# Kernel tuning notes

Hardware: AMD Instinct MI355X
Metric: run time of the kernel (lower is better)

## Reference

```python
import jax, jax.numpy as jnp
import numpy as np

B, L, DM, H, PD = 2, 1024, 512, 8, 64
D = DM // H  # head_dim = 64
NEG = -10000.0


def setup_inputs() -> dict:
    key = jax.random.key(0)
    ks = jax.random.split(key, 12)
    s = 1.0 / np.sqrt(DM)
    sp = 1.0 / np.sqrt(PD)
    return {
        "x": jax.random.normal(ks[0], (B, L, DM), dtype=jnp.float32),
        "z": jax.random.normal(ks[1], (B, L, L, PD), dtype=jnp.float32),
        "residue_mask": jnp.ones((B, L), dtype=bool),
        "Wq": jax.random.normal(ks[2], (DM, DM), dtype=jnp.float32) * s,
        "bq": jnp.zeros((DM,), dtype=jnp.float32),
        "Wk": jax.random.normal(ks[3], (DM, DM), dtype=jnp.float32) * s,
        "bk": jnp.zeros((DM,), dtype=jnp.float32),
        "Wv": jax.random.normal(ks[4], (DM, DM), dtype=jnp.float32) * s,
        "bv": jnp.zeros((DM,), dtype=jnp.float32),
        "Wo": jax.random.normal(ks[5], (DM, DM), dtype=jnp.float32) * s,
        "bo": jnp.zeros((DM,), dtype=jnp.float32),
        "Wpb": jax.random.normal(ks[6], (PD, H), dtype=jnp.float32) * sp,
    }


def reference(x, z, residue_mask, Wq, bq, Wk, bk, Wv, bv, Wo, bo, Wpb):
    b, l, c = x.shape
    scale = 1.0 / np.sqrt(D)
    # projections -> (B, H, L, D)
    q = (x @ Wq + bq).reshape(b, l, H, D).transpose(0, 2, 1, 3)
    k = (x @ Wk + bk).reshape(b, l, H, D).transpose(0, 2, 1, 3)
    v = (x @ Wv + bv).reshape(b, l, H, D).transpose(0, 2, 1, 3)
    # pair bias: (B, L, L, PD) @ (PD, H) -> (B, H, L, L)
    bias = jnp.einsum('bijp,ph->bhij', z, Wpb)
    logits = jnp.einsum('bhid,bhjd->bhij', q, k) * scale + bias
    key_ok = residue_mask[:, None, None, :]
    query_ok = residue_mask[:, None, :, None]
    logits = jnp.where(key_ok, logits, NEG)
    logits = jnp.where(query_ok, logits, NEG)
    attn = jax.nn.softmax(logits, axis=-1)
    out = jnp.einsum('bhij,bhjd->bhid', attn, v)
    out = out.transpose(0, 2, 1, 3).reshape(b, l, c)
    return out @ Wo + bo
```

## Files before the change

kernel.cpp:

```cpp
#include <hip/hip_runtime.h>

typedef __bf16 bf16;
typedef __attribute__((ext_vector_type(4))) __bf16 bf16x4;
typedef __attribute__((ext_vector_type(8))) __bf16 bf16x8;
typedef __attribute__((ext_vector_type(4))) float f32x4;
typedef __attribute__((ext_vector_type(4))) _Float16 f16x4;
typedef __attribute__((ext_vector_type(2))) _Float16 f16x2;

#define B_   2
#define L_   1024
#define DM_  512
#define H_   8
#define D_   64
#define PD_  64
#define NEG_VAL -10000.0f

#define WTPB_N (16*64)

static __device__ __forceinline__ f32x4 mfma_bf16(bf16x8 a, bf16x8 b, f32x4 c) {
  return __builtin_amdgcn_mfma_f32_16x16x32_bf16(a, b, c, 0, 0, 0);
}

__global__ __launch_bounds__(256) void prep_kernel(
    const float* __restrict__ x, const float* __restrict__ Wq, const float* __restrict__ Wk,
    const float* __restrict__ Wv, const float* __restrict__ Wo, const float* __restrict__ Wpb,
    bf16* __restrict__ xb, bf16* __restrict__ Wt, bf16* __restrict__ Wto, bf16* __restrict__ Wtpb) {
  __shared__ float td[32][33];
  int bid = blockIdx.x, tid = threadIdx.x;
  if (bid < 1024) {
    int r = tid >> 3, c4 = (tid & 7) * 4;
    const float* src;
    bf16* dstbase;
    int n0, k0, srcol;
    if (bid < 768) {
      int nt2 = bid >> 4, kt = bid & 15;
      n0 = nt2 * 32; k0 = kt * 32;
      int sel = n0 >> 9;
      src = sel == 0 ? Wq : (sel == 1 ? Wk : Wv);
      srcol = n0 & 511;
      dstbase = Wt + (long)n0 * 512;
    } else {
      int t2 = bid - 768;
      int nt2 = t2 >> 4, kt = t2 & 15;
      n0 = nt2 * 32; k0 = kt * 32;
      src = Wo; srcol = n0;
      dstbase = Wto + (long)n0 * 512;
    }
    f32x4 v = *reinterpret_cast<const f32x4*>(src + (long)(k0 + r) * 512 + srcol + c4);
#pragma unroll
    for (int e = 0; e < 4; ++e) td[r][c4 + e] = v[e];
    __syncthreads();
    int nl = tid >> 3, k4 = (tid & 7) * 4;
    bf16x4 o;
#pragma unroll
    for (int e = 0; e < 4; ++e) o[e] = (bf16)td[k4 + e][nl];
    *reinterpret_cast<bf16x4*>(dstbase + (long)nl * 512 + k0 + k4) = o;
  } else if (bid < 2048) {
    int base = (bid - 1024) * 1024 + tid * 4;
    f32x4 v = *reinterpret_cast<const f32x4*>(x + base);
    bf16x4 o;
#pragma unroll
    for (int e = 0; e < 4; ++e) o[e] = (bf16)v[e];
    *reinterpret_cast<bf16x4*>(xb + base) = o;
  } else {
    for (int t = tid; t < WTPB_N; t += 256) {
      int n = t >> 6, kk = t & 63;
      Wtpb[t] = (n < 8) ? (bf16)Wpb[kk * 8 + n] : (bf16)0.0f;
    }
  }
}

__global__ __launch_bounds__(256) void qkv_gemm(
    const bf16* __restrict__ xb, const bf16* __restrict__ Wt,
    const float* __restrict__ bq, const float* __restrict__ bk, const float* __restrict__ bv,
    bf16* __restrict__ qb, bf16* __restrict__ kb, bf16* __restrict__ vT) {
  int wid = blockIdx.x * 4 + (threadIdx.x >> 6);
  int lane = threadIdx.x & 63;
  int mt = wid / 48, nt = wid - mt * 48;
  int row0 = mt * 32, col0 = nt * 32;
  int lr = lane & 15, lg = lane >> 4;
  const bf16* a0p = xb + (row0 + lr) * 512 + lg * 8;
  const bf16* a1p = a0p + 16 * 512;
  const bf16* b0p = Wt + (col0 + lr) * 512 + lg * 8;
  const bf16* b1p = b0p + 16 * 512;
  f32x4 acc00 = {0.f,0.f,0.f,0.f}, acc01 = acc00, acc10 = acc00, acc11 = acc00;
#pragma unroll
  for (int kk = 0; kk < 512; kk += 32) {
    bf16x8 a0 = *reinterpret_cast<const bf16x8*>(a0p + kk);
    bf16x8 a1 = *reinterpret_cast<const bf16x8*>(a1p + kk);
    bf16x8 b0 = *reinterpret_cast<const bf16x8*>(b0p + kk);
    bf16x8 b1 = *reinterpret_cast<const bf16x8*>(b1p + kk);
    acc00 = mfma_bf16(a0, b0, acc00);
    acc01 = mfma_bf16(a0, b1, acc01);
    acc10 = mfma_bf16(a1, b0, acc10);
    acc11 = mfma_bf16(a1, b1, acc11);
  }
#pragma unroll
  for (int ni = 0; ni < 2; ++ni) {
    int col = col0 + ni * 16 + lr;
    int wsel = col >> 9;
    int ncol = col & 511;
    int h = ncol >> 6, d = ncol & 63;
    const float* bias = wsel == 0 ? bq : (wsel == 1 ? bk : bv);
    float bval = bias[ncol];
#pragma unroll
    for (int mi = 0; mi < 2; ++mi) {
      f32x4 acc = (mi == 0) ? (ni == 0 ? acc00 : acc01) : (ni == 0 ? acc10 : acc11);
      int m0 = row0 + mi * 16 + lg * 4;
      int bidx = m0 >> 10, l0 = m0 & 1023;
      if (wsel == 2) {
        bf16x4 pv;
#pragma unroll
        for (int r = 0; r < 4; ++r) pv[r] = (bf16)(acc[r] + bval);
        *reinterpret_cast<bf16x4*>(vT + ((long)(bidx * H_ + h) * D_ + d) * L_ + l0) = pv;
      } else if (wsel == 0) {
#pragma unroll
        for (int r = 0; r < 4; ++r)
          qb[((long)(bidx * H_ + h) * L_ + l0 + r) * D_ + d] = (bf16)((acc[r] + bval) * 0.125f);
      } else {
#pragma unroll
        for (int r = 0; r < 4; ++r)
          kb[((long)(bidx * H_ + h) * L_ + l0 + r) * D_ + d] = (bf16)(acc[r] + bval);
      }
    }
  }
}

__global__ __launch_bounds__(256) void bias_gemm(
    const float* __restrict__ z, const bf16* __restrict__ Wtpb, const int* __restrict__ mask,
    _Float16* __restrict__ biasbuf) {
  __shared__ float zt_raw[64 * 64];
  __shared__ _Float16 bt[8][72];
  int tid = threadIdx.x;
  int w = tid >> 6, lane = tid & 63;
  int lr = lane & 15, lg = lane >> 4;
  char* zb = (char*)zt_raw;
  const char* zsrc = (const char*)(z + (long)blockIdx.x * 4096);
#pragma unroll
  for (int q = 0; q < 4; ++q) {
    int lb = q * 4096 + tid * 16;
    int row = lb >> 8, col = lb & 255;
    f32x4 v = *reinterpret_cast<const f32x4*>(zsrc + lb);
    *reinterpret_cast<f32x4*>(zb + row * 256 + (col ^ ((row & 7) << 5))) = v;
  }
  bf16x8 b0 = *reinterpret_cast<const bf16x8*>(Wtpb + lr * 64 + lg * 8);
  bf16x8 b1 = *reinterpret_cast<const bf16x8*>(Wtpb + lr * 64 + 32 + lg * 8);
  __syncthreads();
  int row = w * 16 + lr;
  int sw = (row & 7) << 5;
  const char* zr = zb + row * 256;
  f32x4 z0 = *reinterpret_cast<const f32x4*>(zr + ((lg * 32) ^ sw));
  f32x4 z1 = *reinterpret_cast<const f32x4*>(zr + (((lg * 32) ^ sw) + 16));
  f32x4 z2 = *reinterpret_cast<const f32x4*>(zr + ((128 + lg * 32) ^ sw));
  f32x4 z3 = *reinterpret_cast<const f32x4*>(zr + (((128 + lg * 32) ^ sw) + 16));
  bf16x8 a0, a1;
#pragma unroll
  for (int e = 0; e < 4; ++e) { a0[e] = (bf16)z0[e]; a0[e + 4] = (bf16)z1[e]; }
#pragma unroll
  for (int e = 0; e < 4; ++e) { a1[e] = (bf16)z2[e]; a1[e + 4] = (bf16)z3[e]; }
  f32x4 acc = {0.f, 0.f, 0.f, 0.f};
  acc = mfma_bf16(a0, b0, acc);
  acc = mfma_bf16(a1, b1, acc);
  __syncthreads();
  if (lr < 8) {
    f16x4 hv;
#pragma unroll
    for (int r = 0; r < 4; ++r) hv[r] = (_Float16)acc[r];
    *reinterpret_cast<f16x4*>(&bt[lr][w * 16 + lg * 4]) = hv;
  }
  __syncthreads();
  {
    int h = tid >> 5, part = tid & 31;
    long pb = (long)blockIdx.x * 64;
    int b = (int)(pb >> 20), i = ((int)(pb >> 10)) & 1023, j0 = (int)pb & 1023;
    int j = j0 + part * 2;
    f16x2 v = *reinterpret_cast<const f16x2*>(&bt[h][part * 2]);
    if (mask[b * L_ + j] == 0)     v[0] = (_Float16)NEG_VAL;
    if (mask[b * L_ + j + 1] == 0) v[1] = (_Float16)NEG_VAL;
    _Float16* dst = biasbuf + ((((long)b * H_ + h) * L_ + i) << 10) + j;
    *reinterpret_cast<f16x2*>(dst) = v;
  }
}

__global__ __launch_bounds__(256) void attn_kernel(
    const bf16* __restrict__ qb, const bf16* __restrict__ kb, const bf16* __restrict__ vT,
    const _Float16* __restrict__ biasb, const int* __restrict__ mask, bf16* __restrict__ attn_out) {
  __shared__ bf16 p_lds[4][16 * 64];
  __shared__ float o_lds[4][16][64];
  __shared__ float m_lds[4][16];
  __shared__ float l_lds[4][16];
  int bid = blockIdx.x;
  int b = bid >> 9, h = (bid >> 6) & 7, it = bid & 63;
  int i0 = it * 16;
  int tid = threadIdx.x, w = tid >> 6, lane = tid & 63, lr = lane & 15, lg = lane >> 4;

  const bf16* qrow = qb + ((long)(b * H_ + h) * L_ + i0 + lr) * D_ + lg * 8;
  bf16x8 qa0 = *reinterpret_cast<const bf16x8*>(qrow);
  bf16x8 qa1 = *reinterpret_cast<const bf16x8*>(qrow + 32);
  const bf16* kbase = kb + (long)(b * H_ + h) * L_ * D_;
  const bf16* vbase = vT + (long)(b * H_ + h) * D_ * L_;
  const _Float16* bias_base = biasb + ((long)(b * H_ + h) * L_ + i0) * L_;
  bool qok = mask[b * L_ + i0 + lr] != 0;

  float m = -3.0e38f, l = 0.f;
  f32x4 o0 = {0.f,0.f,0.f,0.f}, o1 = o0, o2 = o0, o3 = o0;
  char* pbuf = (char*)&p_lds[w][0];
  int swz = (lr & 7) << 4;

  for (int jt = 0; jt < 4; ++jt) {
    int j0 = w * 256 + jt * 64;
    f32x4 s0, s1, s2, s3;
#pragma unroll
    for (int tile = 0; tile < 4; ++tile) {
      f16x4 bv = *reinterpret_cast<const f16x4*>(bias_base + (long)lr * L_ + j0 + tile * 16 + lg * 4);
      f32x4 acc;
#pragma unroll
      for (int r = 0; r < 4; ++r) acc[r] = (float)bv[r];
      const bf16* kr = kbase + (long)(j0 + tile * 16 + lr) * D_ + lg * 8;
      acc = mfma_bf16(*reinterpret_cast<const bf16x8*>(kr), qa0, acc);
      acc = mfma_bf16(*reinterpret_cast<const bf16x8*>(kr + 32), qa1, acc);
      if (tile == 0) s0 = acc; else if (tile == 1) s1 = acc; else if (tile == 2) s2 = acc; else s3 = acc;
    }
    if (!qok) {
#pragma unroll
      for (int r = 0; r < 4; ++r) { s0[r] = NEG_VAL; s1[r] = NEG_VAL; s2[r] = NEG_VAL; s3[r] = NEG_VAL; }
    }
    float mt = s0[0];
#pragma unroll
    for (int r = 0; r < 4; ++r) mt = fmaxf(fmaxf(fmaxf(mt, s0[r]), fmaxf(s1[r], s2[r])), s3[r]);
    mt = fmaxf(mt, __shfl_xor(mt, 16));
    mt = fmaxf(mt, __shfl_xor(mt, 32));
    float mnew = fmaxf(m, mt);
    float alpha = __expf(m - mnew);
    m = mnew;
    f32x4 p0, p1, p2, p3;
    float ps = 0.f;
#pragma unroll
    for (int r = 0; r < 4; ++r) {
      p0[r] = __expf(s0[r] - mnew); p1[r] = __expf(s1[r] - mnew);
      p2[r] = __expf(s2[r] - mnew); p3[r] = __expf(s3[r] - mnew);
      ps += p0[r] + p1[r] + p2[r] + p3[r];
    }
    ps += __shfl_xor(ps, 16);
    ps += __shfl_xor(ps, 32);
    l = l * alpha + ps;
#pragma unroll
    for (int r = 0; r < 4; ++r) { o0[r] *= alpha; o1[r] *= alpha; o2[r] *= alpha; o3[r] *= alpha; }
#pragma unroll
    for (int tile = 0; tile < 4; ++tile) {
      f32x4 pv = (tile == 0) ? p0 : (tile == 1) ? p1 : (tile == 2) ? p2 : p3;
      bf16x4 pb_;
#pragma unroll
      for (int r = 0; r < 4; ++r) pb_[r] = (bf16)pv[r];
      *reinterpret_cast<bf16x4*>(pbuf + ((lr * 128 + tile * 32 + lg * 8) ^ swz)) = pb_;
    }
    bf16x8 pa0 = *reinterpret_cast<const bf16x8*>(pbuf + ((lr * 128 + lg * 16) ^ swz));
    bf16x8 pa1 = *reinterpret_cast<const bf16x8*>(pbuf + ((lr * 128 + 64 + lg * 16) ^ swz));
#pragma unroll
    for (int dtile = 0; dtile < 4; ++dtile) {
      const bf16* vr = vbase + (long)(dtile * 16 + lr) * L_ + j0 + lg * 8;
      f32x4 acc = (dtile == 0) ? o0 : (dtile == 1) ? o1 : (dtile == 2) ? o2 : o3;
      acc = mfma_bf16(*reinterpret_cast<const bf16x8*>(vr), pa0, acc);
      acc = mfma_bf16(*reinterpret_cast<const bf16x8*>(vr + 32), pa1, acc);
      if (dtile == 0) o0 = acc; else if (dtile == 1) o1 = acc; else if (dtile == 2) o2 = acc; else o3 = acc;
    }
  }
#pragma unroll
  for (int dtile = 0; dtile < 4; ++dtile) {
    f32x4 ov = (dtile == 0) ? o0 : (dtile == 1) ? o1 : (dtile == 2) ? o2 : o3;
    *reinterpret_cast<f32x4*>(&o_lds[w][lr][dtile * 16 + lg * 4]) = ov;
  }
  if (lg == 0) { m_lds[w][lr] = m; l_lds[w][lr] = l; }
  __syncthreads();
  {
    int row = tid >> 4, d0 = (tid & 15) * 4;
    float M = fmaxf(fmaxf(m_lds[0][row], m_lds[1][row]), fmaxf(m_lds[2][row], m_lds[3][row]));
    float lt = 0.f;
    float oacc[4] = {0.f, 0.f, 0.f, 0.f};
#pragma unroll
    for (int ww = 0; ww < 4; ++ww) {
      float c = __expf(m_lds[ww][row] - M);
      lt += c * l_lds[ww][row];
#pragma unroll
      for (int e = 0; e < 4; ++e) oacc[e] += c * o_lds[ww][row][d0 + e];
    }
    float inv = 1.0f / lt;
    bf16x4 ov;
#pragma unroll
    for (int e = 0; e < 4; ++e) ov[e] = (bf16)(oacc[e] * inv);
    *reinterpret_cast<bf16x4*>(attn_out + ((long)(b * L_ + i0 + row)) * DM_ + h * D_ + d0) = ov;
  }
}

__global__ __launch_bounds__(64) void out_gemm(
    const bf16* __restrict__ ab, const bf16* __restrict__ Wto,
    const float* __restrict__ bo, float* __restrict__ out) {
  int wid = blockIdx.x;
  int lane = threadIdx.x;
  int mt = wid >> 4, nt = wid & 15;
  int row0 = mt * 32, col0 = nt * 32;
  int lr = lane & 15, lg = lane >> 4;
  const bf16* a0p = ab + (row0 + lr) * 512 + lg * 8;
  const bf16* a1p = a0p + 16 * 512;
  const bf16* b0p = Wto + (col0 + lr) * 512 + lg * 8;
  const bf16* b1p = b0p + 16 * 512;
  f32x4 acc00 = {0.f,0.f,0.f,0.f}, acc01 = acc00, acc10 = acc00, acc11 = acc00;
#pragma unroll
  for (int kk = 0; kk < 512; kk += 32) {
    bf16x8 a0 = *reinterpret_cast<const bf16x8*>(a0p + kk);
    bf16x8 a1 = *reinterpret_cast<const bf16x8*>(a1p + kk);
    bf16x8 b0 = *reinterpret_cast<const bf16x8*>(b0p + kk);
    bf16x8 b1 = *reinterpret_cast<const bf16x8*>(b1p + kk);
    acc00 = mfma_bf16(a0, b0, acc00);
    acc01 = mfma_bf16(a0, b1, acc01);
    acc10 = mfma_bf16(a1, b0, acc10);
    acc11 = mfma_bf16(a1, b1, acc11);
  }
#pragma unroll
  for (int ni = 0; ni < 2; ++ni) {
    int col = col0 + ni * 16 + lr;
    float bval = bo[col];
#pragma unroll
    for (int mi = 0; mi < 2; ++mi) {
      f32x4 acc = (mi == 0) ? (ni == 0 ? acc00 : acc01) : (ni == 0 ? acc10 : acc11);
      int m0 = row0 + mi * 16 + lg * 4;
#pragma unroll
      for (int r = 0; r < 4; ++r) out[(long)(m0 + r) * 512 + col] = acc[r] + bval;
    }
  }
}

extern "C" void kernel_launch(void* const* d_in, const int* in_sizes, int n_in,
                              void* d_out, int out_size, void* d_ws, size_t ws_size,
                              hipStream_t stream) {
  const float* x    = (const float*)d_in[0];
  const float* z    = (const float*)d_in[1];
  const int*   mask = (const int*)d_in[2];
  const float* Wq   = (const float*)d_in[3];
  const float* bq   = (const float*)d_in[4];
  const float* Wk   = (const float*)d_in[5];
  const float* bk   = (const float*)d_in[6];
  const float* Wv   = (const float*)d_in[7];
  const float* bv   = (const float*)d_in[8];
  const float* Wo   = (const float*)d_in[9];
  const float* bo   = (const float*)d_in[10];
  const float* Wpb  = (const float*)d_in[11];

  char* ws = (char*)d_ws;
  bf16* xb        = (bf16*)(ws + 0);
  bf16* Wt        = (bf16*)(ws + 2097152);
  bf16* Wto       = (bf16*)(ws + 3670016);
  bf16* Wtpb      = (bf16*)(ws + 4194304);
  bf16* qbuf      = (bf16*)(ws + 4196352);
  bf16* kbuf      = (bf16*)(ws + 6293504);
  bf16* vTbuf     = (bf16*)(ws + 8390656);
  bf16* attn_out  = (bf16*)(ws + 10487808);
  _Float16* biasb = (_Float16*)(ws + 12584960);

  prep_kernel<<<2049, 256, 0, stream>>>(x, Wq, Wk, Wv, Wo, Wpb, xb, Wt, Wto, Wtpb);
  qkv_gemm<<<768, 256, 0, stream>>>(xb, Wt, bq, bk, bv, qbuf, kbuf, vTbuf);
  bias_gemm<<<32768, 256, 0, stream>>>(z, Wtpb, mask, biasb);
  attn_kernel<<<1024, 256, 0, stream>>>(qbuf, kbuf, vTbuf, biasb, mask, attn_out);
  out_gemm<<<1024, 64, 0, stream>>>(attn_out, Wto, bo, (float*)d_out);
}
```

Before: 192.6 us.

## Tile bias GEMM over 16x64 blocks and store bias in MFMA-fragment layout

The pair-bias kernel now processes a 16-row by 64-column tile of z per block, 2048 blocks instead of 32768. It reads z directly from global memory into MFMA fragments, with no LDS staging. It writes the bias in a tiled layout that matches the attention kernel's per-lane fragment reads, so attention loads are contiguous per tile, and the mask is applied with vectorized loads. The output GEMM packs four waves per block instead of one-wave blocks. The aim is to cut launch and block overhead and the poorly coalesced bias traffic. The cost is a custom intermediate layout shared between the two kernels, and direct z loads that are strided per lane.

New measurement: 193.7 us. About the same (+0.6%).

```diff
diff --git a/kernel.cpp b/kernel.cpp
--- a/kernel.cpp
+++ b/kernel.cpp
@@ -129,56 +129,52 @@
 __global__ __launch_bounds__(256) void bias_gemm(
     const float* __restrict__ z, const bf16* __restrict__ Wtpb, const int* __restrict__ mask,
     _Float16* __restrict__ biasbuf) {
-  __shared__ float zt_raw[64 * 64];
-  __shared__ _Float16 bt[8][72];
-  int tid = threadIdx.x;
-  int w = tid >> 6, lane = tid & 63;
+  __shared__ _Float16 outt[8][1032];
+  int tid = threadIdx.x, w = tid >> 6, lane = tid & 63;
   int lr = lane & 15, lg = lane >> 4;
-  char* zb = (char*)zt_raw;
-  const char* zsrc = (const char*)(z + (long)blockIdx.x * 4096);
-#pragma unroll
-  for (int q = 0; q < 4; ++q) {
-    int lb = q * 4096 + tid * 16;
-    int row = lb >> 8, col = lb & 255;
-    f32x4 v = *reinterpret_cast<const f32x4*>(zsrc + lb);
-    *reinterpret_cast<f32x4*>(zb + row * 256 + (col ^ ((row & 7) << 5))) = v;
-  }
-  bf16x8 b0 = *reinterpret_cast<const bf16x8*>(Wtpb + lr * 64 + lg * 8);
-  bf16x8 b1 = *reinterpret_cast<const bf16x8*>(Wtpb + lr * 64 + 32 + lg * 8);
-  __syncthreads();
-  int row = w * 16 + lr;
-  int sw = (row & 7) << 5;
-  const char* zr = zb + row * 256;
-  f32x4 z0 = *reinterpret_cast<const f32x4*>(zr + ((lg * 32) ^ sw));
-  f32x4 z1 = *reinterpret_cast<const f32x4*>(zr + (((lg * 32) ^ sw) + 16));
-  f32x4 z2 = *reinterpret_cast<const f32x4*>(zr + ((128 + lg * 32) ^ sw));
-  f32x4 z3 = *reinterpret_cast<const f32x4*>(zr + (((128 + lg * 32) ^ sw) + 16));
-  bf16x8 a0, a1;
-#pragma unroll
-  for (int e = 0; e < 4; ++e) { a0[e] = (bf16)z0[e]; a0[e + 4] = (bf16)z1[e]; }
-#pragma unroll
-  for (int e = 0; e < 4; ++e) { a1[e] = (bf16)z2[e]; a1[e + 4] = (bf16)z3[e]; }
-  f32x4 acc = {0.f, 0.f, 0.f, 0.f};
-  acc = mfma_bf16(a0, b0, acc);
-  acc = mfma_bf16(a1, b1, acc);
-  __syncthreads();
-  if (lr < 8) {
-    f16x4 hv;
-#pragma unroll
-    for (int r = 0; r < 4; ++r) hv[r] = (_Float16)acc[r];
-    *reinterpret_cast<f16x4*>(&bt[lr][w * 16 + lg * 4]) = hv;
+  int bid = blockIdx.x;
+  int jc = bid & 15, it = (bid >> 4) & 63, b = bid >> 10;
+  bf16x8 wb0 = *reinterpret_cast<const bf16x8*>(Wtpb + lr * 64 + lg * 8);
+  bf16x8 wb1 = *reinterpret_cast<const bf16x8*>(Wtpb + lr * 64 + 32 + lg * 8);
+#pragma unroll
+  for (int ii = 0; ii < 4; ++ii) {
+    int il = w * 4 + ii;
+    int i = it * 16 + il;
+#pragma unroll
+    for (int js = 0; js < 4; ++js) {
+      const float* zr = z + ((long)(b * L_ + i) * L_ + jc * 64 + js * 16 + lr) * 64 + lg * 8;
+      f32x4 z0 = *reinterpret_cast<const f32x4*>(zr);
+      f32x4 z1 = *reinterpret_cast<const f32x4*>(zr + 4);
+      f32x4 z2 = *reinterpret_cast<const f32x4*>(zr + 32);
+      f32x4 z3 = *reinterpret_cast<const f32x4*>(zr + 36);
+      bf16x8 a0, a1;
+#pragma unroll
+      for (int e = 0; e < 4; ++e) {
+        a0[e] = (bf16)z0[e]; a0[e + 4] = (bf16)z1[e];
+        a1[e] = (bf16)z2[e]; a1[e + 4] = (bf16)z3[e];
+      }
+      f32x4 c = {0.f, 0.f, 0.f, 0.f};
+      c = mfma_bf16(a0, wb0, c);
+      c = mfma_bf16(a1, wb1, c);
+      if (lr < 8) {
+        int4 mk = *reinterpret_cast<const int4*>(mask + b * L_ + jc * 64 + js * 16 + lg * 4);
+        f16x4 hv;
+        hv[0] = mk.x ? (_Float16)c[0] : (_Float16)NEG_VAL;
+        hv[1] = mk.y ? (_Float16)c[1] : (_Float16)NEG_VAL;
+        hv[2] = mk.z ? (_Float16)c[2] : (_Float16)NEG_VAL;
+        hv[3] = mk.w ? (_Float16)c[3] : (_Float16)NEG_VAL;
+        *reinterpret_cast<f16x4*>(&outt[lr][((js * 4 + lg) * 16 + il) * 4]) = hv;
+      }
+    }
   }
   __syncthreads();
   {
-    int h = tid >> 5, part = tid & 31;
-    long pb = (long)blockIdx.x * 64;
-    int b = (int)(pb >> 20), i = ((int)(pb >> 10)) & 1023, j0 = (int)pb & 1023;
-    int j = j0 + part * 2;
-    f16x2 v = *reinterpret_cast<const f16x2*>(&bt[h][part * 2]);
-    if (mask[b * L_ + j] == 0)     v[0] = (_Float16)NEG_VAL;
-    if (mask[b * L_ + j + 1] == 0) v[1] = (_Float16)NEG_VAL;
-    _Float16* dst = biasbuf + ((((long)b * H_ + h) * L_ + i) << 10) + j;
-    *reinterpret_cast<f16x2*>(dst) = v;
+    int h = tid & 7, part = tid >> 3;
+    _Float16* dst = biasbuf + (((((long)b * H_ + h) * 64 + it) * 16 + jc) << 10) + part * 32;
+    const _Float16* srcl = &outt[h][part * 32];
+#pragma unroll
+    for (int e = 0; e < 8; ++e)
+      *reinterpret_cast<f16x4*>(dst + e * 4) = *reinterpret_cast<const f16x4*>(srcl + e * 4);
   }
 }
 
@@ -199,7 +195,7 @@
   bf16x8 qa1 = *reinterpret_cast<const bf16x8*>(qrow + 32);
   const bf16* kbase = kb + (long)(b * H_ + h) * L_ * D_;
   const bf16* vbase = vT + (long)(b * H_ + h) * D_ * L_;
-  const _Float16* bias_base = biasb + ((long)(b * H_ + h) * L_ + i0) * L_;
+  const _Float16* bias_base = biasb + ((((long)(b * H_ + h) * 64 + it)) << 14);
   bool qok = mask[b * L_ + i0 + lr] != 0;
 
   float m = -3.0e38f, l = 0.f;
@@ -209,10 +205,11 @@
 
   for (int jt = 0; jt < 4; ++jt) {
     int j0 = w * 256 + jt * 64;
+    const _Float16* btile = bias_base + ((w * 4 + jt) << 10);
     f32x4 s0, s1, s2, s3;
 #pragma unroll
     for (int tile = 0; tile < 4; ++tile) {
-      f16x4 bv = *reinterpret_cast<const f16x4*>(bias_base + (long)lr * L_ + j0 + tile * 16 + lg * 4);
+      f16x4 bv = *reinterpret_cast<const f16x4*>(btile + ((tile * 4 + lg) * 16 + lr) * 4);
       f32x4 acc;
 #pragma unroll
       for (int r = 0; r < 4; ++r) acc[r] = (float)bv[r];
@@ -292,11 +289,11 @@
   }
 }
 
-__global__ __launch_bounds__(64) void out_gemm(
+__global__ __launch_bounds__(256) void out_gemm(
     const bf16* __restrict__ ab, const bf16* __restrict__ Wto,
     const float* __restrict__ bo, float* __restrict__ out) {
-  int wid = blockIdx.x;
-  int lane = threadIdx.x;
+  int wid = blockIdx.x * 4 + (threadIdx.x >> 6);
+  int lane = threadIdx.x & 63;
   int mt = wid >> 4, nt = wid & 15;
   int row0 = mt * 32, col0 = nt * 32;
   int lr = lane & 15, lg = lane >> 4;
@@ -359,7 +356,7 @@
 
   prep_kernel<<<2049, 256, 0, stream>>>(x, Wq, Wk, Wv, Wo, Wpb, xb, Wt, Wto, Wtpb);
   qkv_gemm<<<768, 256, 0, stream>>>(xb, Wt, bq, bk, bv, qbuf, kbuf, vTbuf);
-  bias_gemm<<<32768, 256, 0, stream>>>(z, Wtpb, mask, biasb);
+  bias_gemm<<<2048, 256, 0, stream>>>(z, Wtpb, mask, biasb);
   attn_kernel<<<1024, 256, 0, stream>>>(qbuf, kbuf, vTbuf, biasb, mask, attn_out);
-  out_gemm<<<1024, 64, 0, stream>>>(attn_out, Wto, bo, (float*)d_out);
-}
+  out_gemm<<<256, 256, 0, stream>>>(attn_out, Wto, bo, (float*)d_out);
+}
```
